# Optimization experiments

Hardware: AMD Instinct MI355X
Metric: run time of the kernel (lower is better)

Reference implementation:

```python
import math
import jax, jax.numpy as jnp
import numpy as np

D_MODEL = 2048
NUM_HEADS = 16
HEAD_DIM = 128
MIN_PERIOD = 0.01
MAX_PERIOD = 10.0
LN_EPS = 1e-5


def temporal_pos_enc(num_frames, frame_interval, d_model, dtype):
    # frame times in seconds, sin-cos encoding with log-spaced periods.
    times = jnp.arange(num_frames, dtype=jnp.float32) * frame_interval  # [N]
    fraction = jnp.linspace(0.0, 1.0, d_model // 2, dtype=jnp.float32)  # [D/2]
    period = MIN_PERIOD * (MAX_PERIOD / MIN_PERIOD) ** fraction
    scaling = (2.0 * math.pi) / period                                  # [D/2]
    sin_in = times[:, None] * scaling[None, :]                          # [N, D/2]
    enc = jnp.concatenate([jnp.sin(sin_in), jnp.cos(sin_in)], axis=1)   # [N, D]
    return enc.astype(dtype)


def setup_inputs() -> dict:
    key = jax.random.key(0)
    ks = jax.random.split(key, 7)
    B, N, S, L_other, D = 4, 4, 768, 48, D_MODEL
    HD = NUM_HEADS * HEAD_DIM
    seq_len = N * S + L_other
    scale = 1.0 / math.sqrt(D)
    return {
        "hidden_states": jax.random.normal(ks[0], (B, seq_len, D), jnp.float32),
        "Wq": jax.random.normal(ks[1], (HD, D), jnp.float32) * scale,
        "Wk": jax.random.normal(ks[2], (HD, D), jnp.float32) * scale,
        "Wv": jax.random.normal(ks[3], (HD, D), jnp.float32) * scale,
        "Wo": jax.random.normal(ks[4], (D, HD), jnp.float32) * scale,
        "ln_gamma": jnp.ones((D,), jnp.float32),
        "ln_beta": jnp.zeros((D,), jnp.float32),
        "num_image_tokens_per_frame": 768,
        "num_frames": 4,
        "frame_interval": 0.1,
    }


def reference(hidden_states, Wq, Wk, Wv, Wo, ln_gamma, ln_beta,
              num_image_tokens_per_frame, num_frames, frame_interval):
    B, seq_len, D = hidden_states.shape
    S = num_image_tokens_per_frame
    N = num_frames
    T = S * N
    H, hd = NUM_HEADS, HEAD_DIM
    scaling = hd ** (-0.5)

    img = hidden_states[:, :T, :]           # [B, T, D]
    other = hidden_states[:, T:, :]         # [B, L_other, D]
    residual = img

    # fp32 LayerNorm
    x32 = img.astype(jnp.float32)
    mu = jnp.mean(x32, axis=-1, keepdims=True)
    var = jnp.mean(jnp.square(x32 - mu), axis=-1, keepdims=True)
    x = ((x32 - mu) * jax.lax.rsqrt(var + LN_EPS) * ln_gamma + ln_beta).astype(hidden_states.dtype)

    # [B, N, S, D] + temporal pos enc broadcast over batch & space
    x = x.reshape(B, N, S, D)
    x = x + temporal_pos_enc(N, frame_interval, D, x.dtype)[None, :, None, :]
    x = jnp.transpose(x, (0, 2, 1, 3))      # [B, S, N, D]

    # QKV projections (Linear: y = x @ W.T)
    q = jnp.einsum('bsnd,ed->bsne', x, Wq).reshape(B, S, N, H, hd)
    k = jnp.einsum('bsnd,ed->bsne', x, Wk).reshape(B, S, N, H, hd)
    v = jnp.einsum('bsnd,ed->bsne', x, Wv).reshape(B, S, N, H, hd)

    # attention over temporal axis (n, m are frame indices)
    scores = jnp.einsum('bsnhd,bsmhd->bshnm', q, k) * scaling
    attn = jax.nn.softmax(scores.astype(jnp.float32), axis=-1).astype(q.dtype)
    out = jnp.einsum('bshnm,bsmhd->bsnhd', attn, v)   # [B, S, N, H, hd]
    out = out.reshape(B, S, N, H * hd)
    out = jnp.einsum('bsne,de->bsnd', out, Wo)        # [B, S, N, D]

    out = jnp.transpose(out, (0, 2, 1, 3)).reshape(B, N * S, D)
    img_out = residual + out
    return jnp.concatenate([img_out, other], axis=1)
```

## Files before the change

### kernel.cpp

```cpp
#include <hip/hip_runtime.h>
#include <hip/hip_bf16.h>
#include <math.h>

#define BATCH 4
#define NFRM  4
#define STOK  768
#define TIMG  3072
#define SEQ   3120
#define DM    2048
#define NH    16
#define HDIM  128
#define MTOK  12288

typedef __attribute__((ext_vector_type(8))) short short8;
typedef __attribute__((ext_vector_type(4))) float f32x4;

__device__ __forceinline__ unsigned short f2bf(float f) {
  unsigned u = __float_as_uint(f);
  u += 0x7FFF + ((u >> 16) & 1);
  return (unsigned short)(u >> 16);
}
__device__ __forceinline__ float bf2f(unsigned short s) {
  return __uint_as_float(((unsigned)s) << 16);
}

__device__ __forceinline__ void gload_lds16(const void* g, void* l) {
  __builtin_amdgcn_global_load_lds(
      (const __attribute__((address_space(1))) void*)g,
      (__attribute__((address_space(3))) void*)l,
      16, 0, 0);
}

__device__ __forceinline__ void barrier_fenced() {
  asm volatile("" ::: "memory");
  __builtin_amdgcn_s_barrier();
  asm volatile("" ::: "memory");
}

__global__ void k_enc(const float* __restrict__ fi, float* __restrict__ enc) {
  int i = blockIdx.x * 256 + threadIdx.x;
  if (i >= NFRM * DM) return;
  int n = i >> 11;
  int d = i & (DM - 1);
  int dd = d & 1023;
  float fraction = dd * (1.0f / 1023.0f);
  float period = 0.01f * powf(1000.0f, fraction);
  float sc = 6.283185307179586f / period;
  float x = (n * fi[0]) * sc;
  enc[i] = (d < 1024) ? sinf(x) : cosf(x);
}

__global__ void k_wconv(const float4* __restrict__ Wq, const float4* __restrict__ Wk,
                        const float4* __restrict__ Wv, const float4* __restrict__ Wo,
                        unsigned short* __restrict__ wqkv, unsigned short* __restrict__ wo) {
  int id = blockIdx.x * 256 + threadIdx.x;
  int mat = id >> 20;
  int j = id & 1048575;
  const float4* src = (mat == 0) ? Wq : (mat == 1) ? Wk : (mat == 2) ? Wv : Wo;
  float4 v = src[j];
  ushort4 o4;
  o4.x = f2bf(v.x); o4.y = f2bf(v.y); o4.z = f2bf(v.z); o4.w = f2bf(v.w);
  unsigned short* dst = (mat < 3) ? (wqkv + (size_t)mat * 4194304) : wo;
  *(ushort4*)&dst[(size_t)j * 4] = o4;
}

__global__ __launch_bounds__(256)
void k_ln(const float* __restrict__ hid, const float* __restrict__ gamma,
          const float* __restrict__ beta, const float* __restrict__ enc,
          unsigned short* __restrict__ X) {
  int token = blockIdx.x;
  int b = token / TIMG;
  int t = token - b * TIMG;
  int n = t / STOK;
  const float* row = hid + (size_t)(b * SEQ + t) * DM;
  int tid = threadIdx.x;

  float xv[8];
  *(float4*)&xv[0] = *(const float4*)&row[tid * 8];
  *(float4*)&xv[4] = *(const float4*)&row[tid * 8 + 4];

  float s = 0.f, ss = 0.f;
#pragma unroll
  for (int j = 0; j < 8; ++j) { s += xv[j]; ss += xv[j] * xv[j]; }
#pragma unroll
  for (int mask = 32; mask >= 1; mask >>= 1) {
    s += __shfl_xor(s, mask);
    ss += __shfl_xor(ss, mask);
  }
  __shared__ float ps[4], pss[4];
  int lane = tid & 63, wid = tid >> 6;
  if (lane == 0) { ps[wid] = s; pss[wid] = ss; }
  __syncthreads();
  s = ps[0] + ps[1] + ps[2] + ps[3];
  ss = pss[0] + pss[1] + pss[2] + pss[3];

  float mean = s * (1.0f / DM);
  float var = ss * (1.0f / DM) - mean * mean;
  float inv = rsqrtf(var + 1e-5f);

  float gv[8], bv[8], ev[8];
  *(float4*)&gv[0] = *(const float4*)&gamma[tid * 8];
  *(float4*)&gv[4] = *(const float4*)&gamma[tid * 8 + 4];
  *(float4*)&bv[0] = *(const float4*)&beta[tid * 8];
  *(float4*)&bv[4] = *(const float4*)&beta[tid * 8 + 4];
  *(float4*)&ev[0] = *(const float4*)&enc[n * DM + tid * 8];
  *(float4*)&ev[4] = *(const float4*)&enc[n * DM + tid * 8 + 4];

  short8 outv;
#pragma unroll
  for (int j = 0; j < 8; ++j) {
    float y = (xv[j] - mean) * inv * gv[j] + bv[j] + ev[j];
    outv[j] = (short)f2bf(y);
  }
  *(short8*)&X[(size_t)token * DM + tid * 8] = outv;
}

template <int EPI>
__global__ __launch_bounds__(512, 2)
void gemm256(const unsigned short* __restrict__ A, const unsigned short* __restrict__ B,
             unsigned short* __restrict__ Cb, float* __restrict__ Cf,
             const float* __restrict__ resid, int M, int N, int K, int nbx) {
  __shared__ char lds[131072];

  const int nwg = gridDim.x;
  const int q = nwg >> 3;
  const int bid = blockIdx.x;
  const int swz = (bid & 7) * q + (bid >> 3);
  const int by = swz / nbx;
  const int bx = swz - by * nbx;
  const int tm = by * 256, tn = bx * 256;

  const int tid = threadIdx.x;
  const int lane = tid & 63;
  const int wid = tid >> 6;
  const int wm = wid >> 2;
  const int wn = wid & 3;
  const int l16 = lane & 15;
  const int kq = lane >> 4;

  const int srow = tid >> 3;
  const int sslot = tid & 7;
  const unsigned short* gA[4];
  const unsigned short* gB[4];
#pragma unroll
  for (int i = 0; i < 4; ++i) {
    int row = i * 64 + srow;
    int lslot = sslot ^ (row & 7);
    gA[i] = A + (size_t)(tm + row) * K + lslot * 8;
    gB[i] = B + (size_t)(tn + row) * K + lslot * 8;
  }

  f32x4 acc[8][4];
#pragma unroll
  for (int i = 0; i < 8; ++i)
#pragma unroll
    for (int j = 0; j < 4; ++j) acc[i][j] = (f32x4){0.f, 0.f, 0.f, 0.f};

  auto STAGE = [&](int k0, int buf) {
    char* base = lds + buf * 65536 + wid * 1024;
#pragma unroll
    for (int i = 0; i < 4; ++i) gload_lds16(gA[i] + k0, base + i * 8192);
#pragma unroll
    for (int i = 0; i < 4; ++i) gload_lds16(gB[i] + k0, base + 32768 + i * 8192);
  };

  auto COMPUTE = [&](int buf) {
    const char* pa = lds + buf * 65536;
    const char* pb = pa + 32768;
    short8 breg[4][2];
#pragma unroll
    for (int ni = 0; ni < 4; ++ni)
#pragma unroll
      for (int ks = 0; ks < 2; ++ks) {
        int row = wn * 64 + ni * 16 + l16;
        int slot = (ks * 4 + kq) ^ (row & 7);
        breg[ni][ks] = *(const short8*)(pb + row * 128 + slot * 16);
      }
#pragma unroll
    for (int p = 0; p < 4; ++p) {
      short8 areg[2][2];
#pragma unroll
      for (int mi = 0; mi < 2; ++mi)
#pragma unroll
        for (int ks = 0; ks < 2; ++ks) {
          int row = wm * 128 + (p * 2 + mi) * 16 + l16;
          int slot = (ks * 4 + kq) ^ (row & 7);
          areg[mi][ks] = *(const short8*)(pa + row * 128 + slot * 16);
        }
      __builtin_amdgcn_s_setprio(1);
#pragma unroll
      for (int mi = 0; mi < 2; ++mi)
#pragma unroll
        for (int ni = 0; ni < 4; ++ni)
#pragma unroll
          for (int ks = 0; ks < 2; ++ks)
            acc[p * 2 + mi][ni] = __builtin_amdgcn_mfma_f32_16x16x32_bf16(
                areg[mi][ks], breg[ni][ks], acc[p * 2 + mi][ni], 0, 0, 0);
      __builtin_amdgcn_s_setprio(0);
    }
  };

  const int NT = K >> 6;
  STAGE(0, 0);
  for (int t = 0; t < NT - 1; ++t) {
    STAGE((t + 1) << 6, (t + 1) & 1);
    asm volatile("s_waitcnt vmcnt(8)" ::: "memory");
    barrier_fenced();
    COMPUTE(t & 1);
    barrier_fenced();
  }
  asm volatile("s_waitcnt vmcnt(0)" ::: "memory");
  barrier_fenced();
  COMPUTE((NT - 1) & 1);

#pragma unroll
  for (int mi = 0; mi < 8; ++mi) {
#pragma unroll
    for (int ni = 0; ni < 4; ++ni) {
      int row0 = tm + wm * 128 + mi * 16 + kq * 4;
      int col = tn + wn * 64 + ni * 16 + l16;
#pragma unroll
      for (int r = 0; r < 4; ++r) {
        int row = row0 + r;
        float val = acc[mi][ni][r];
        if (EPI == 0) {
          Cb[(size_t)row * N + col] = f2bf(val);
        } else {
          int bb = row / TIMG;
          int t2 = row - bb * TIMG;
          size_t o = (size_t)(bb * SEQ + t2) * DM + col;
          Cf[o] = resid[o] + val;
        }
      }
    }
  }
}

__global__ __launch_bounds__(256)
void k_attn(const unsigned short* __restrict__ QKV, unsigned short* __restrict__ AOUT) {
  int bs = blockIdx.x;
  int b = bs / STOK;
  int s = bs - b * STOK;
  int tid = threadIdx.x;
  int h = tid >> 4;
  int part = tid & 15;
  int col = h * HDIM + part * 8;

  float q[4][8], k[4][8], v[4][8];
#pragma unroll
  for (int n = 0; n < 4; ++n) {
    size_t base = (size_t)(b * TIMG + n * STOK + s) * 6144;
    short8 qa = *(const short8*)&QKV[base + col];
    short8 ka = *(const short8*)&QKV[base + 2048 + col];
    short8 va = *(const short8*)&QKV[base + 4096 + col];
#pragma unroll
    for (int j = 0; j < 8; ++j) {
      q[n][j] = bf2f((unsigned short)qa[j]);
      k[n][j] = bf2f((unsigned short)ka[j]);
      v[n][j] = bf2f((unsigned short)va[j]);
    }
  }

  float sc[4][4];
#pragma unroll
  for (int n = 0; n < 4; ++n)
#pragma unroll
    for (int m = 0; m < 4; ++m) {
      float a = 0.f;
#pragma unroll
      for (int j = 0; j < 8; ++j) a += q[n][j] * k[m][j];
#pragma unroll
      for (int mask = 8; mask >= 1; mask >>= 1) a += __shfl_xor(a, mask);
      sc[n][m] = a * 0.08838834764831845f;
    }

  float p[4][4];
#pragma unroll
  for (int n = 0; n < 4; ++n) {
    float mx = fmaxf(fmaxf(sc[n][0], sc[n][1]), fmaxf(sc[n][2], sc[n][3]));
    float sum = 0.f;
#pragma unroll
    for (int m = 0; m < 4; ++m) { p[n][m] = expf(sc[n][m] - mx); sum += p[n][m]; }
    float inv = 1.f / sum;
#pragma unroll
    for (int m = 0; m < 4; ++m) p[n][m] *= inv;
  }

#pragma unroll
  for (int n = 0; n < 4; ++n) {
    float o[8];
#pragma unroll
    for (int j = 0; j < 8; ++j) o[j] = 0.f;
#pragma unroll
    for (int m = 0; m < 4; ++m)
#pragma unroll
      for (int j = 0; j < 8; ++j) o[j] += p[n][m] * v[m][j];
    short8 ov;
#pragma unroll
    for (int j = 0; j < 8; ++j) ov[j] = (short)f2bf(o[j]);
    size_t obase = (size_t)(b * TIMG + n * STOK + s) * DM + col;
    *(short8*)&AOUT[obase] = ov;
  }
}

__global__ void k_other(const float4* __restrict__ hid, float4* __restrict__ out) {
  int i = blockIdx.x * 256 + threadIdx.x;
  int b = i / 24576;
  int r = i - b * 24576;
  size_t off = ((size_t)(b * SEQ + TIMG) * DM) / 4 + r;
  out[off] = hid[off];
}

extern "C" void kernel_launch(void* const* d_in, const int* in_sizes, int n_in,
                              void* d_out, int out_size, void* d_ws, size_t ws_size,
                              hipStream_t stream) {
  const float* hid   = (const float*)d_in[0];
  const float* Wq    = (const float*)d_in[1];
  const float* Wk    = (const float*)d_in[2];
  const float* Wv    = (const float*)d_in[3];
  const float* Wo    = (const float*)d_in[4];
  const float* gamma = (const float*)d_in[5];
  const float* beta  = (const float*)d_in[6];
  const float* fint  = (const float*)d_in[9];
  float* out = (float*)d_out;

  char* ws = (char*)d_ws;
  float*          enc  = (float*)(ws + 0);
  unsigned short* wqkv = (unsigned short*)(ws + 32768);
  unsigned short* wo   = (unsigned short*)(ws + 25198592);
  unsigned short* X    = (unsigned short*)(ws + 33587200);
  unsigned short* QKV  = (unsigned short*)(ws + 83918848);
  unsigned short* aout = X;

  k_enc<<<32, 256, 0, stream>>>(fint, enc);
  k_wconv<<<16384, 256, 0, stream>>>((const float4*)Wq, (const float4*)Wk,
                                     (const float4*)Wv, (const float4*)Wo, wqkv, wo);
  k_ln<<<MTOK, 256, 0, stream>>>(hid, gamma, beta, enc, X);
  gemm256<0><<<1152, 512, 0, stream>>>(X, wqkv, QKV, nullptr, nullptr,
                                       MTOK, 6144, DM, 24);
  k_attn<<<BATCH * STOK, 256, 0, stream>>>(QKV, aout);
  gemm256<1><<<384, 512, 0, stream>>>(aout, wo, nullptr, out, hid,
                                      MTOK, DM, DM, 8);
  k_other<<<384, 256, 0, stream>>>((const float4*)hid, (float4*)out);
}
```

Before: 705.7 us.

## Restructure GEMM main loop into four-quadrant ping-pong with split half-tile prefetch

Replaces the stage-then-compute double-buffered GEMM loop with a schedule that splits each 256x256 tile into four quadrant MFMA phases. Global-to-LDS loads for the next tiles are issued in halves, interleaved between phases, and the B tile is prefetched two iterations ahead. The goal is to overlap LDS reads, global loads and MFMA work more finely and to keep the matrix units busy. In exchange it adds many more barriers per iteration and relies on careful vmcnt accounting across buffers, which risks stalls or race bugs.

```diff
diff --git a/kernel.cpp b/kernel.cpp
--- a/kernel.cpp
+++ b/kernel.cpp
@@ -29,12 +29,6 @@
       (const __attribute__((address_space(1))) void*)g,
       (__attribute__((address_space(3))) void*)l,
       16, 0, 0);
-}
-
-__device__ __forceinline__ void barrier_fenced() {
-  asm volatile("" ::: "memory");
-  __builtin_amdgcn_s_barrier();
-  asm volatile("" ::: "memory");
 }
 
 __global__ void k_enc(const float* __restrict__ fi, float* __restrict__ enc) {
@@ -140,15 +134,19 @@
 
   const int srow = tid >> 3;
   const int sslot = tid & 7;
-  const unsigned short* gA[4];
-  const unsigned short* gB[4];
-#pragma unroll
-  for (int i = 0; i < 4; ++i) {
-    int row = i * 64 + srow;
-    int lslot = sslot ^ (row & 7);
-    gA[i] = A + (size_t)(tm + row) * K + lslot * 8;
-    gB[i] = B + (size_t)(tn + row) * K + lslot * 8;
-  }
+  const unsigned short* baseA = A + (size_t)(tm + srow) * K + (sslot ^ (srow & 7)) * 8;
+  const unsigned short* baseB = B + (size_t)(tn + srow) * K + (sslot ^ (srow & 7)) * 8;
+
+  const int NT = K >> 6;
+
+  auto SHALF = [&](int tile, int mat, int half) {
+    if (tile >= NT) return;
+    char* dst = lds + (tile & 1) * 65536 + mat * 32768 + half * 16384 + wid * 1024;
+    const unsigned short* src =
+        (mat == 0 ? baseA : baseB) + (size_t)(half * 128) * K + tile * 64;
+    gload_lds16(src, dst);
+    gload_lds16(src + (size_t)64 * K, dst + 8192);
+  };
 
   f32x4 acc[8][4];
 #pragma unroll
@@ -156,62 +154,114 @@
 #pragma unroll
     for (int j = 0; j < 4; ++j) acc[i][j] = (f32x4){0.f, 0.f, 0.f, 0.f};
 
-  auto STAGE = [&](int k0, int buf) {
-    char* base = lds + buf * 65536 + wid * 1024;
-#pragma unroll
-    for (int i = 0; i < 4; ++i) gload_lds16(gA[i] + k0, base + i * 8192);
-#pragma unroll
-    for (int i = 0; i < 4; ++i) gload_lds16(gB[i] + k0, base + 32768 + i * 8192);
-  };
-
-  auto COMPUTE = [&](int buf) {
-    const char* pa = lds + buf * 65536;
+  SHALF(0, 0, 0); SHALF(0, 0, 1); SHALF(0, 1, 0); SHALF(0, 1, 1);
+  SHALF(1, 1, 0); SHALF(1, 1, 1);
+  asm volatile("s_waitcnt vmcnt(4)" ::: "memory");
+  __builtin_amdgcn_sched_barrier(0);
+  __builtin_amdgcn_s_barrier();
+
+  short8 a0[4][2], a1[4][2], b0[2][2], b1[2][2];
+
+  for (int t = 0; t < NT; ++t) {
+    const char* pa = lds + (t & 1) * 65536;
     const char* pb = pa + 32768;
-    short8 breg[4][2];
-#pragma unroll
-    for (int ni = 0; ni < 4; ++ni)
+
+#pragma unroll
+    for (int mi = 0; mi < 4; ++mi)
 #pragma unroll
       for (int ks = 0; ks < 2; ++ks) {
-        int row = wn * 64 + ni * 16 + l16;
-        int slot = (ks * 4 + kq) ^ (row & 7);
-        breg[ni][ks] = *(const short8*)(pb + row * 128 + slot * 16);
-      }
-#pragma unroll
-    for (int p = 0; p < 4; ++p) {
-      short8 areg[2][2];
-#pragma unroll
-      for (int mi = 0; mi < 2; ++mi)
-#pragma unroll
-        for (int ks = 0; ks < 2; ++ks) {
-          int row = wm * 128 + (p * 2 + mi) * 16 + l16;
-          int slot = (ks * 4 + kq) ^ (row & 7);
-          areg[mi][ks] = *(const short8*)(pa + row * 128 + slot * 16);
-        }
-      __builtin_amdgcn_s_setprio(1);
-#pragma unroll
-      for (int mi = 0; mi < 2; ++mi)
-#pragma unroll
-        for (int ni = 0; ni < 4; ++ni)
-#pragma unroll
-          for (int ks = 0; ks < 2; ++ks)
-            acc[p * 2 + mi][ni] = __builtin_amdgcn_mfma_f32_16x16x32_bf16(
-                areg[mi][ks], breg[ni][ks], acc[p * 2 + mi][ni], 0, 0, 0);
-      __builtin_amdgcn_s_setprio(0);
+        int r = wm * 128 + mi * 16 + l16;
+        a0[mi][ks] = *(const short8*)(pa + r * 128 + (((ks * 4 + kq) ^ (r & 7)) * 16));
+      }
+#pragma unroll
+    for (int ni = 0; ni < 2; ++ni)
+#pragma unroll
+      for (int ks = 0; ks < 2; ++ks) {
+        int r = wn * 64 + ni * 16 + l16;
+        b0[ni][ks] = *(const short8*)(pb + r * 128 + (((ks * 4 + kq) ^ (r & 7)) * 16));
+      }
+    SHALF(t + 1, 0, 0);
+    __builtin_amdgcn_s_barrier();
+    asm volatile("s_waitcnt lgkmcnt(0)" ::: "memory");
+    __builtin_amdgcn_sched_barrier(0);
+    __builtin_amdgcn_s_setprio(1);
+#pragma unroll
+    for (int mi = 0; mi < 4; ++mi)
+#pragma unroll
+      for (int ni = 0; ni < 2; ++ni)
+#pragma unroll
+        for (int ks = 0; ks < 2; ++ks)
+          acc[mi][ni] = __builtin_amdgcn_mfma_f32_16x16x32_bf16(
+              a0[mi][ks], b0[ni][ks], acc[mi][ni], 0, 0, 0);
+    __builtin_amdgcn_s_setprio(0);
+    __builtin_amdgcn_s_barrier();
+
+#pragma unroll
+    for (int ni = 0; ni < 2; ++ni)
+#pragma unroll
+      for (int ks = 0; ks < 2; ++ks) {
+        int r = wn * 64 + (ni + 2) * 16 + l16;
+        b1[ni][ks] = *(const short8*)(pb + r * 128 + (((ks * 4 + kq) ^ (r & 7)) * 16));
+      }
+    SHALF(t + 1, 0, 1);
+    __builtin_amdgcn_s_barrier();
+    asm volatile("s_waitcnt lgkmcnt(0)" ::: "memory");
+    __builtin_amdgcn_sched_barrier(0);
+    __builtin_amdgcn_s_setprio(1);
+#pragma unroll
+    for (int mi = 0; mi < 4; ++mi)
+#pragma unroll
+      for (int ni = 0; ni < 2; ++ni)
+#pragma unroll
+        for (int ks = 0; ks < 2; ++ks)
+          acc[mi][ni + 2] = __builtin_amdgcn_mfma_f32_16x16x32_bf16(
+              a0[mi][ks], b1[ni][ks], acc[mi][ni + 2], 0, 0, 0);
+    __builtin_amdgcn_s_setprio(0);
+    __builtin_amdgcn_s_barrier();
+
+#pragma unroll
+    for (int mi = 0; mi < 4; ++mi)
+#pragma unroll
+      for (int ks = 0; ks < 2; ++ks) {
+        int r = wm * 128 + (mi + 4) * 16 + l16;
+        a1[mi][ks] = *(const short8*)(pa + r * 128 + (((ks * 4 + kq) ^ (r & 7)) * 16));
+      }
+    SHALF(t + 2, 1, 0);
+    __builtin_amdgcn_s_barrier();
+    asm volatile("s_waitcnt lgkmcnt(0)" ::: "memory");
+    __builtin_amdgcn_sched_barrier(0);
+    __builtin_amdgcn_s_setprio(1);
+#pragma unroll
+    for (int mi = 0; mi < 4; ++mi)
+#pragma unroll
+      for (int ni = 0; ni < 2; ++ni)
+#pragma unroll
+        for (int ks = 0; ks < 2; ++ks)
+          acc[mi + 4][ni + 2] = __builtin_amdgcn_mfma_f32_16x16x32_bf16(
+              a1[mi][ks], b1[ni][ks], acc[mi + 4][ni + 2], 0, 0, 0);
+    __builtin_amdgcn_s_setprio(0);
+    __builtin_amdgcn_s_barrier();
+
+    SHALF(t + 2, 1, 1);
+    if (t + 2 < NT) {
+      asm volatile("s_waitcnt vmcnt(4)" ::: "memory");
+    } else {
+      asm volatile("s_waitcnt vmcnt(0)" ::: "memory");
     }
-  };
-
-  const int NT = K >> 6;
-  STAGE(0, 0);
-  for (int t = 0; t < NT - 1; ++t) {
-    STAGE((t + 1) << 6, (t + 1) & 1);
-    asm volatile("s_waitcnt vmcnt(8)" ::: "memory");
-    barrier_fenced();
-    COMPUTE(t & 1);
-    barrier_fenced();
-  }
-  asm volatile("s_waitcnt vmcnt(0)" ::: "memory");
-  barrier_fenced();
-  COMPUTE((NT - 1) & 1);
+    __builtin_amdgcn_sched_barrier(0);
+    __builtin_amdgcn_s_barrier();
+    __builtin_amdgcn_s_setprio(1);
+#pragma unroll
+    for (int mi = 0; mi < 4; ++mi)
+#pragma unroll
+      for (int ni = 0; ni < 2; ++ni)
+#pragma unroll
+        for (int ks = 0; ks < 2; ++ks)
+          acc[mi + 4][ni] = __builtin_amdgcn_mfma_f32_16x16x32_bf16(
+              a1[mi][ks], b0[ni][ks], acc[mi + 4][ni], 0, 0, 0);
+    __builtin_amdgcn_s_setprio(0);
+    __builtin_amdgcn_s_barrier();
+  }
 
 #pragma unroll
   for (int mi = 0; mi < 8; ++mi) {
```

New measurement: 707.3 us. Within noise of the previous version (+0.2%).
